# Kernel optimization log

Hardware: AMD Instinct MI355X
Metric: run time of the kernel (lower is better)

Reference implementation:

```python
import jax, jax.numpy as jnp
import numpy as np

N, IN_DIM, HID, OUT, NH = 512, 256, 256, 256, 4
HD = OUT // NH  # head_dim = 64
EPS = 1e-5


def _mlp(x, w1, b1, w2, b2):
    return jax.nn.relu(x @ w1 + b1) @ w2 + b2


def setup_inputs() -> dict:
    key = jax.random.key(0)
    ks = jax.random.split(key, 32)

    def rn(k, shape, fan_in):
        return (jax.random.normal(k, shape, jnp.float32) / np.float32(np.sqrt(fan_in)))

    V = jax.random.normal(ks[0], (N, IN_DIM), jnp.float32)
    adj = jax.random.randint(ks[1], (N, N), 0, 2, jnp.int32)
    adj = adj.at[jnp.arange(N), jnp.arange(N)].set(1)  # self-edges: avoid all -inf rows
    prev_hidden = jax.random.normal(ks[2], (N, HID), jnp.float32)
    z = jnp.zeros
    return dict(
        V=V, adj=adj, prev_hidden=prev_hidden,
        W1=rn(ks[3], (IN_DIM, HID), IN_DIM),
        a_std0=rn(ks[4], (HID, 1), HID), a_std1=rn(ks[5], (HID, 1), HID),
        ce_w1=rn(ks[6], (2 * IN_DIM, HID), 2 * IN_DIM), ce_b1=z((HID,), jnp.float32),
        ce_w2=rn(ks[7], (HID, HD), HID), ce_b2=z((HD,), jnp.float32),
        a_c0=rn(ks[8], (HD, 1), HD), a_c1=rn(ks[9], (HD, 1), HD),
        te_w1=rn(ks[10], (IN_DIM + HID, HID), IN_DIM + HID), te_b1=z((HID,), jnp.float32),
        te_w2=rn(ks[11], (HID, HD), HID), te_b2=z((HD,), jnp.float32),
        a_t0=rn(ks[12], (HD, 1), HD), a_t1=rn(ks[13], (HD, 1), HD),
        co_w1=rn(ks[14], (3 * IN_DIM, HID), 3 * IN_DIM), co_b1=z((HID,), jnp.float32),
        co_w2=rn(ks[15], (HID, HD), HID), co_b2=z((HD,), jnp.float32),
        a_co0=rn(ks[16], (HD, 1), HD), a_co1=rn(ks[17], (HD, 1), HD),
        W2=rn(ks[18], (HID + 2 * HD + 1, OUT), HID + 2 * HD + 1),
        Wo=rn(ks[19], (OUT, OUT), OUT), bo=z((OUT,), jnp.float32),
        ln_g=jnp.ones((OUT,), jnp.float32), ln_b=z((OUT,), jnp.float32),
    )


def reference(V, adj, prev_hidden, W1, a_std0, a_std1,
              ce_w1, ce_b1, ce_w2, ce_b2, a_c0, a_c1,
              te_w1, te_b1, te_w2, te_b2, a_t0, a_t1,
              co_w1, co_b1, co_w2, co_b2, a_co0, a_co1,
              W2, Wo, bo, ln_g, ln_b):
    ninf = -jnp.inf

    # ---- standard GAT branch -> H1: (N, HID) ----
    Wh1 = V @ W1
    s1 = Wh1 @ a_std0 + (Wh1 @ a_std1).T                      # (N, N)
    s1 = jnp.where(adj == 0, ninf, s1)
    H1 = jax.nn.softmax(s1, axis=1) @ Wh1

    # ---- causal branch: all ordered pairs i!=j, global softmax -> H2: (N, HD) ----
    pair = jnp.concatenate([jnp.broadcast_to(V[:, None, :], (N, N, IN_DIM)),
                            jnp.broadcast_to(V[None, :, :], (N, N, IN_DIM))], axis=-1)
    cf = _mlp(pair, ce_w1, ce_b1, ce_w2, ce_b2)               # (N, N, HD)
    cs = (cf @ (a_c0 + a_c1))[..., 0]                         # (N, N)
    cs = jnp.where(jnp.eye(N, dtype=bool), ninf, cs)          # exclude i==j pairs
    ca = jax.nn.softmax(cs.reshape(-1)).reshape(N, N, 1)
    H2 = jnp.broadcast_to((ca * cf).sum((0, 1)), (N, HD))

    # ---- temporal branch: (N,1) scores broadcast against causal mask -> running mean ----
    tf = _mlp(jnp.concatenate([V, prev_hidden], axis=-1), te_w1, te_b1, te_w2, te_b2)  # (N, HD)
    ts = tf @ (a_t0 + a_t1)                                   # (N, 1)
    cmask = jnp.triu(jnp.ones((N, N), bool), 1)
    tsb = jnp.where(cmask, ninf, jnp.broadcast_to(ts, (N, N)))
    H3 = jax.nn.softmax(tsb, axis=1) @ tf                     # (N, HD)

    # ---- coop branch: first two neighbors by index; size-1 softmax; buggy pad -> (N,1) ----
    order = jnp.argsort((1 - adj).astype(jnp.int32), axis=1, stable=True)  # adj==1 first, index order
    nb = V[order[:, :2]]                                      # (N, 2, IN_DIM)
    valid = ((adj == 1).sum(axis=1) >= 2)
    nb = jnp.where(valid[:, None, None], nb, jnp.zeros_like(nb))
    ci = jnp.concatenate([V, nb[:, 0], nb[:, 1]], axis=-1)    # (N, 3*IN_DIM)
    cf4 = _mlp(ci, co_w1, co_b1, co_w2, co_b2)                # (N, HD)
    ca4 = jax.nn.softmax(cf4 @ (a_co0 + a_co1), axis=1)       # (N,1): softmax over size-1 -> ones
    h4vec = (ca4.T @ cf4)[0]                                  # (HD,)
    # original: squeeze(-2)->(HD,), dim==1 -> unsqueeze(-1)->(HD,1), zero-pad rows to N
    H4 = jnp.zeros((N, 1), V.dtype).at[:HD, 0].set(h4vec)

    # ---- combine, lazy W2, proj, LN, ELU (dropout identity in eval) ----
    Hc = jnp.concatenate([H1, H2, H3, H4], axis=-1) @ W2      # (N, OUT)
    out = Hc @ Wo + bo
    mu = out.mean(-1, keepdims=True)
    var = ((out - mu) ** 2).mean(-1, keepdims=True)
    out = (out - mu) / jnp.sqrt(var + EPS) * ln_g + ln_b
    return jax.nn.elu(out)
```

## Files before the change

kernel.cpp:

```cpp
#include <hip/hip_runtime.h>
#include <math.h>

#define NN 512
#define HD 64
#define EPSV 1e-5f

typedef unsigned short u16;
typedef short s4v __attribute__((ext_vector_type(4)));
typedef short s8v __attribute__((ext_vector_type(8)));
typedef float f4v __attribute__((ext_vector_type(4)));

struct GD {
  const float *A, *A2, *A3, *A4;
  const int* I;
  const float *B, *bias;
  float* C;
  int M, K, Nn, mode, act;
};

#define GEMM_SMEM 28800
#define MEGA_SMEM 38656

__device__ __forceinline__ void split_bf16(float x, u16& h, u16& l) {
  unsigned xb = __float_as_uint(x);
  float hf = __uint_as_float(xb & 0xffff0000u);
  h = (u16)(xb >> 16);
  l = (u16)(__float_as_uint(x - hf) >> 16);
}

__device__ __forceinline__ void gemm_body(char* smem, const GD& d, int bx, int by) {
  u16 (*Ah)[72] = (u16(*)[72])smem;
  u16 (*Al)[72] = (u16(*)[72])(smem + 4608);
  u16 (*Bh)[68] = (u16(*)[68])(smem + 9216);
  u16 (*Bl)[68] = (u16(*)[68])(smem + 9216 + 8704);
  char* extra = smem + 26624;
  int* nbl = (int*)extra;
  float* wscl = (float*)extra;
  float* rowsuml = wscl + 512;

  const int t = threadIdx.x;
  const int rowbase = by * 32, colbase = bx * 64;
  const int K = d.K, Nn = d.Nn, mode = d.mode, M = d.M;
  if (rowbase >= M) return;

  if (mode == 2) {
    int wave = t >> 6, lane = t & 63;
    for (int rr = wave; rr < 32; rr += 4) {
      int row = rowbase + rr;
      int n0 = -1, n1 = -1, cnt = 0;
      for (int c = 0; c < 8; ++c) {
        unsigned long long mm = __ballot(d.I[row * NN + c * 64 + lane] != 0);
        cnt += (int)__popcll(mm);
        if (n0 < 0 && mm) { n0 = c * 64 + (int)__builtin_ctzll(mm); mm &= mm - 1; }
        if (n1 < 0 && mm) { n1 = c * 64 + (int)__builtin_ctzll(mm); }
      }
      if (lane == 0) { nbl[rr * 3] = n0; nbl[rr * 3 + 1] = n1; nbl[rr * 3 + 2] = (cnt >= 2); }
    }
    __syncthreads();
  } else if (mode == 4) {
    wscl[t] = d.A2[t];
    wscl[256 + t] = d.A2[256 + t];
    __syncthreads();
  }

  float4 aR[2], bR[4];
  float rs0 = 0.f, rs1 = 0.f;

  auto loadA = [&](int k0) {
#pragma unroll
    for (int j = 0; j < 2; ++j) {
      int idx = t + j * 256;
      int r = idx >> 4, c0 = (idx & 15) * 4;
      int row = rowbase + r, gk = k0 + c0;
      float4 v4 = make_float4(0.f, 0.f, 0.f, 0.f);
      if (mode == 0) {
        if (row < M && gk < K) v4 = *(const float4*)&d.A[(size_t)row * K + gk];
      } else if (mode == 1) {
        if (gk < 256) v4 = *(const float4*)&d.A[row * 256 + gk];
        else v4 = *(const float4*)&d.A2[row * 256 + gk - 256];
      } else if (mode == 2) {
        int seg = gk >> 8;
        int src = (seg == 0) ? row : (nbl[r * 3 + 2] ? nbl[r * 3 + seg - 1] : -1);
        if (src >= 0) v4 = *(const float4*)&d.A[src * 256 + (gk & 255)];
      } else if (mode == 3) {
        if (gk + 3 < 256) v4 = *(const float4*)&d.A[row * 256 + gk];
        else if (gk >= 256 && gk + 3 < 320) v4 = *(const float4*)&d.A2[gk - 256];
        else if (gk >= 320 && gk + 3 < 384) v4 = *(const float4*)&d.A3[row * 64 + gk - 320];
        else if (gk == 384) v4.x = (row < 64) ? d.A4[row] : 0.f;
      } else {
        int4 a4 = *(const int4*)&d.I[row * NN + gk];
        v4.x = a4.x ? wscl[gk + 0] : 0.f;
        v4.y = a4.y ? wscl[gk + 1] : 0.f;
        v4.z = a4.z ? wscl[gk + 2] : 0.f;
        v4.w = a4.w ? wscl[gk + 3] : 0.f;
        float ss = v4.x + v4.y + v4.z + v4.w;
        if (j == 0) rs0 += ss; else rs1 += ss;
      }
      aR[j] = v4;
    }
  };
  auto loadB = [&](int k0) {
#pragma unroll
    for (int j = 0; j < 4; ++j) {
      int idx = t + j * 256;
      int r = idx >> 4, c0 = (idx & 15) * 4;
      int gk = k0 + r;
      float4 v4 = make_float4(0.f, 0.f, 0.f, 0.f);
      if (gk < K) v4 = *(const float4*)&d.B[(size_t)gk * Nn + colbase + c0];
      bR[j] = v4;
    }
  };
  auto stos = [&]() {
#pragma unroll
    for (int j = 0; j < 2; ++j) {
      int idx = t + j * 256;
      int r = idx >> 4, c0 = (idx & 15) * 4;
      float v[4] = {aR[j].x, aR[j].y, aR[j].z, aR[j].w};
      u16 h[4], l[4];
#pragma unroll
      for (int e = 0; e < 4; ++e) split_bf16(v[e], h[e], l[e]);
      *(short4*)&Ah[r][c0] = make_short4(h[0], h[1], h[2], h[3]);
      *(short4*)&Al[r][c0] = make_short4(l[0], l[1], l[2], l[3]);
    }
#pragma unroll
    for (int j = 0; j < 4; ++j) {
      int idx = t + j * 256;
      int r = idx >> 4, c0 = (idx & 15) * 4;
      float v[4] = {bR[j].x, bR[j].y, bR[j].z, bR[j].w};
#pragma unroll
      for (int e = 0; e < 4; ++e) {
        u16 h, l;
        split_bf16(v[e], h, l);
        Bh[c0 + e][r] = h;
        Bl[c0 + e][r] = l;
      }
    }
  };

  f4v acc0 = {0.f, 0.f, 0.f, 0.f};
  f4v acc1 = {0.f, 0.f, 0.f, 0.f};

  const int w4 = t >> 6;
  const int lrow = t & 15;
  const int lk = ((t & 63) >> 4) * 8;

  int iters = (K + 63) >> 6;
  loadA(0); loadB(0);
  for (int it = 0; it < iters; ++it) {
    stos();
    __syncthreads();
    if (it + 1 < iters) { loadA((it + 1) << 6); loadB((it + 1) << 6); }
    const u16* bhrow = Bh[w4 * 16 + lrow];
    const u16* blrow = Bl[w4 * 16 + lrow];
#pragma unroll
    for (int ks = 0; ks < 2; ++ks) {
      int ko = ks * 32 + lk;
      s4v bh_0 = *(const s4v*)&bhrow[ko];
      s4v bh_1 = *(const s4v*)&bhrow[ko + 4];
      s4v bl_0 = *(const s4v*)&blrow[ko];
      s4v bl_1 = *(const s4v*)&blrow[ko + 4];
      s8v bh = __builtin_shufflevector(bh_0, bh_1, 0, 1, 2, 3, 4, 5, 6, 7);
      s8v bl = __builtin_shufflevector(bl_0, bl_1, 0, 1, 2, 3, 4, 5, 6, 7);
      {
        s8v ah = *(const s8v*)&Ah[lrow][ko];
        s8v al = *(const s8v*)&Al[lrow][ko];
        acc0 = __builtin_amdgcn_mfma_f32_16x16x32_bf16(ah, bh, acc0, 0, 0, 0);
        acc0 = __builtin_amdgcn_mfma_f32_16x16x32_bf16(ah, bl, acc0, 0, 0, 0);
        acc0 = __builtin_amdgcn_mfma_f32_16x16x32_bf16(al, bh, acc0, 0, 0, 0);
      }
      {
        s8v ah = *(const s8v*)&Ah[16 + lrow][ko];
        s8v al = *(const s8v*)&Al[16 + lrow][ko];
        acc1 = __builtin_amdgcn_mfma_f32_16x16x32_bf16(ah, bh, acc1, 0, 0, 0);
        acc1 = __builtin_amdgcn_mfma_f32_16x16x32_bf16(ah, bl, acc1, 0, 0, 0);
        acc1 = __builtin_amdgcn_mfma_f32_16x16x32_bf16(al, bh, acc1, 0, 0, 0);
      }
    }
    __syncthreads();
  }

  if (mode == 4) {
    float a0 = rs0, a1 = rs1;
#pragma unroll
    for (int off = 8; off; off >>= 1) {
      a0 += __shfl_xor(a0, off, 16);
      a1 += __shfl_xor(a1, off, 16);
    }
    if ((t & 15) == 0) { rowsuml[t >> 4] = a0; rowsuml[16 + (t >> 4)] = a1; }
    __syncthreads();
  }

  int col = colbase + w4 * 16 + lrow;
  float bvs = d.bias ? d.bias[col] : 0.f;
  int qrow = ((t & 63) >> 4) * 4;
#pragma unroll
  for (int m = 0; m < 2; ++m) {
#pragma unroll
    for (int q = 0; q < 4; ++q) {
      int lr = m * 16 + qrow + q;
      int row = rowbase + lr;
      if (row >= M) continue;
      float o = (m ? acc1[q] : acc0[q]) + bvs;
      if (d.act) o = fmaxf(o, 0.f);
      if (mode == 4) o *= (1.f / rowsuml[lr]);
      d.C[(size_t)row * Nn + col] = o;
    }
  }
}

__device__ void wsc_body(char* smem, const float* W1, const float* a_std1,
                         const float* V, float* expwsc, int grp) {
  float* asl = (float*)smem;
  float* ul  = asl + 256;
  int t = threadIdx.x;
  asl[t] = a_std1[t];
  __syncthreads();
  {
    float s = 0.f;
    const float* wr = W1 + t * 256;
    for (int h = 0; h < 256; h += 4) {
      float4 w4 = *(const float4*)&wr[h];
      float4 a4 = *(const float4*)&asl[h];
      s += w4.x * a4.x + w4.y * a4.y + w4.z * a4.z + w4.w * a4.w;
    }
    ul[t] = s;
  }
  __syncthreads();
  int wave = t >> 6, lane = t & 63;
  float4 u4 = *(const float4*)&ul[lane * 4];
  int j0 = grp * 128;
  for (int j = j0 + wave; j < j0 + 128; j += 4) {
    float4 v4 = *(const float4*)&V[j * 256 + lane * 4];
    float s = v4.x * u4.x + v4.y * u4.y + v4.z * u4.z + v4.w * u4.w;
#pragma unroll
    for (int off = 32; off; off >>= 1) s += __shfl_xor(s, off, 64);
    if (lane == 0) expwsc[j] = __expf(s);
  }
}

struct GD7 { GD d[7]; };
__global__ __launch_bounds__(256) void gemm7_k(GD7 ds) {
  __shared__ __align__(16) char smem[GEMM_SMEM];
  int z = blockIdx.z;
  if (z == 6) {
    if (blockIdx.y != 0) return;
    wsc_body(smem, ds.d[6].A, ds.d[6].A2, ds.d[6].A3, ds.d[6].C, blockIdx.x);
    return;
  }
  gemm_body(smem, ds.d[z], blockIdx.x, blockIdx.y);
}
__global__ __launch_bounds__(256) void gemm1_k(GD d) {
  __shared__ __align__(16) char smem[GEMM_SMEM];
  gemm_body(smem, d, blockIdx.x, blockIdx.y);
}

__device__ void pair_body(char* smem,
    const float* __restrict__ P, const float* __restrict__ Q,
    const float* __restrict__ b1, const float* __restrict__ ce_w2,
    const float* __restrict__ a_c0, const float* __restrict__ a_c1,
    float* __restrict__ mpart, float* __restrict__ dpart,
    float* __restrict__ spart, int byy, int bxx) {
  float* Pl  = (float*)smem;
  float* Ql  = Pl + 16 * 260;
  float* el  = Ql + 16 * 260;
  float* wcl = el + 16 * 20;
  float* red = wcl + 256;
  float* sk  = red + 256;
  float* sbl = sk + 256;
  int t = threadIdx.x;

  if (t < 64) red[t] = a_c0[t] + a_c1[t];
  __syncthreads();
  {
    float s = 0.f;
    const float* w2r = ce_w2 + t * 64;
#pragma unroll 8
    for (int h = 0; h < 64; ++h) s += w2r[h] * red[h];
    wcl[t] = s;
  }
  int i0 = byy * 16, j0 = bxx * 16;
  for (int e = t; e < 1024; e += 256) {
    int r = e >> 6, c4 = (e & 63) * 4;
    float4 bb = *(const float4*)&b1[c4];
    float4 pv = *(const float4*)&P[(i0 + r) * 256 + c4];
    pv.x += bb.x; pv.y += bb.y; pv.z += bb.z; pv.w += bb.w;
    *(float4*)&Pl[r * 260 + c4] = pv;
    *(float4*)&Ql[r * 260 + c4] = *(const float4*)&Q[(j0 + r) * 256 + c4];
  }
  __syncthreads();

  int a = t >> 4, b = t & 15;
  const float* pr = &Pl[a * 260];
  const float* qr = &Ql[b * 260];
  float4 c4a = make_float4(0.f, 0.f, 0.f, 0.f);
#pragma unroll 8
  for (int k4 = 0; k4 < 64; ++k4) {
    float4 w = *(const float4*)&wcl[k4 * 4];
    float4 p = *(const float4*)&pr[k4 * 4];
    float4 q = *(const float4*)&qr[k4 * 4];
    c4a.x += fmaxf(p.x + q.x, 0.f) * w.x;
    c4a.y += fmaxf(p.y + q.y, 0.f) * w.y;
    c4a.z += fmaxf(p.z + q.z, 0.f) * w.z;
    c4a.w += fmaxf(p.w + q.w, 0.f) * w.w;
  }
  float s = c4a.x + c4a.y + c4a.z + c4a.w;
  if (i0 + a == j0 + b) s = -INFINITY;
  red[t] = s; __syncthreads();
  for (int ss = 128; ss; ss >>= 1) { if (t < ss) red[t] = fmaxf(red[t], red[t + ss]); __syncthreads(); }
  float mb = red[0];
  __syncthreads();
  float e = __expf(s - mb);
  el[a * 20 + b] = e;
  red[t] = e; __syncthreads();
  for (int ss = 128; ss; ss >>= 1) { if (t < ss) red[t] += red[t + ss]; __syncthreads(); }
  float db = red[0];
  __syncthreads();

  float qv[16];
#pragma unroll
  for (int j = 0; j < 16; ++j) qv[j] = Ql[j * 260 + t];
  float rk = 0.f;
#pragma unroll 4
  for (int i = 0; i < 16; ++i) {
    float pv = Pl[i * 260 + t];
    const float* erow = &el[i * 20];
#pragma unroll
    for (int j4 = 0; j4 < 4; ++j4) {
      float4 e4 = *(const float4*)&erow[j4 * 4];
      rk += e4.x * fmaxf(pv + qv[j4 * 4 + 0], 0.f);
      rk += e4.y * fmaxf(pv + qv[j4 * 4 + 1], 0.f);
      rk += e4.z * fmaxf(pv + qv[j4 * 4 + 2], 0.f);
      rk += e4.w * fmaxf(pv + qv[j4 * 4 + 3], 0.f);
    }
  }
  sk[t] = rk;
  __syncthreads();
  {
    int h = t & 63, q = t >> 6;
    float s2 = 0.f;
    for (int k = q * 64; k < q * 64 + 64; ++k) s2 += sk[k] * ce_w2[k * 64 + h];
    sbl[q * 64 + h] = s2;
  }
  __syncthreads();
  int blk = byy * 32 + bxx;
  if (t < 64) spart[blk * 64 + t] = sbl[t] + sbl[64 + t] + sbl[128 + t] + sbl[192 + t];
  if (t == 0) { mpart[blk] = mb; dpart[blk] = db; }
}

struct MegaArgs {
  const float *P, *Q, *b1, *ce_w2, *a_c0, *a_c1;
  float *mpart, *dpart, *spart;
  GD gH1, gTf, gCf;
};

__global__ __launch_bounds__(256) void mega_k(MegaArgs a) {
  __shared__ __align__(16) char smem[MEGA_SMEM];
  int b = blockIdx.x;
  if (b < 64) {
    gemm_body(smem, a.gH1, b & 3, b >> 2);
  } else if (b < 80) {
    gemm_body(smem, a.gTf, 0, b - 64);
  } else if (b < 96) {
    gemm_body(smem, a.gCf, 0, b - 80);
  } else {
    int p = b - 96;
    pair_body(smem, a.P, a.Q, a.b1, a.ce_w2, a.a_c0, a.a_c1,
              a.mpart, a.dpart, a.spart, p >> 5, p & 31);
  }
}

__global__ __launch_bounds__(1024) void mini_k(
    const float* __restrict__ mpart, const float* __restrict__ dpart,
    const float* __restrict__ spart, const float* __restrict__ ce_b2,
    float* __restrict__ H2row,
    const float* __restrict__ tf, float* __restrict__ H3,
    const float* __restrict__ cf4, float* __restrict__ h4vec) {
  __shared__ float A[1024];
  __shared__ float Bsh[1024];
  __shared__ float segsum[16][65];
  int b = blockIdx.x, t = threadIdx.x;
  if (b == 0) {
    float mv = mpart[t];
    A[t] = mv; __syncthreads();
    for (int s = 512; s; s >>= 1) { if (t < s) A[t] = fmaxf(A[t], A[t + s]); __syncthreads(); }
    float M = A[0];
    __syncthreads();
    float e = __expf(mv - M);
    Bsh[t] = e;
    A[t] = e * dpart[t];
    __syncthreads();
    for (int s = 512; s; s >>= 1) { if (t < s) A[t] += A[t + s]; __syncthreads(); }
    float D = A[0];
    __syncthreads();
    int h = t & 63, g = t >> 6;
    float s2 = 0.f;
    for (int b2 = g * 64; b2 < g * 64 + 64; ++b2) s2 += Bsh[b2] * spart[b2 * 64 + h];
    A[t] = s2;
    __syncthreads();
    for (int p = 8; p; p >>= 1) { if (g < p) A[g * 64 + h] += A[(g + p) * 64 + h]; __syncthreads(); }
    if (t < 64) H2row[t] = A[t] / D + ce_b2[t];
  } else if (b == 1) {
    int h = t & 63, g = t >> 6;
    float vals[32];
    float run = 0.f;
#pragma unroll
    for (int r = 0; r < 32; ++r) { run += tf[(g * 32 + r) * 64 + h]; vals[r] = run; }
    segsum[g][h] = run;
    __syncthreads();
    float off = 0.f;
    for (int gg = 0; gg < g; ++gg) off += segsum[gg][h];
#pragma unroll
    for (int r = 0; r < 32; ++r) {
      int i = g * 32 + r;
      H3[i * 64 + h] = (vals[r] + off) / (float)(i + 1);
    }
  } else {
    int h = t & 63, g = t >> 6;
    float s = 0.f;
    for (int r = 0; r < 32; ++r) s += cf4[(g * 32 + r) * 64 + h];
    A[g * 64 + h] = s;
    __syncthreads();
    for (int p = 8; p; p >>= 1) { if (g < p) A[g * 64 + h] += A[(g + p) * 64 + h]; __syncthreads(); }
    if (t < 64) h4vec[t] = A[t];
  }
}

__global__ void ln_elu_kernel(const float* __restrict__ X, const float* __restrict__ g,
                              const float* __restrict__ b, float* __restrict__ out) {
  __shared__ float red[256];
  int i = blockIdx.x, tid = threadIdx.x;
  float x = X[i * 256 + tid];
  red[tid] = x; __syncthreads();
  for (int s = 128; s; s >>= 1) { if (tid < s) red[tid] += red[tid + s]; __syncthreads(); }
  float mu = red[0] * (1.f / 256.f);
  __syncthreads();
  float d = x - mu;
  red[tid] = d * d; __syncthreads();
  for (int s = 128; s; s >>= 1) { if (tid < s) red[tid] += red[tid + s]; __syncthreads(); }
  float var = red[0] * (1.f / 256.f);
  float y = d / sqrtf(var + EPSV) * g[tid] + b[tid];
  out[i * 256 + tid] = (y > 0.f) ? y : (expf(y) - 1.f);
}

static GD mkgd(const float* A, const float* A2, const float* A3, const float* A4,
               const int* I, const float* B, const float* bias, float* C,
               int M, int K, int Nn, int mode, int act) {
  GD g{A, A2, A3, A4, I, B, bias, C, M, K, Nn, mode, act};
  return g;
}

extern "C" void kernel_launch(void* const* d_in, const int* in_sizes, int n_in,
                              void* d_out, int out_size, void* d_ws, size_t ws_size,
                              hipStream_t stream) {
  const float* V      = (const float*)d_in[0];
  const int*   adj    = (const int*)  d_in[1];
  const float* ph     = (const float*)d_in[2];
  const float* W1     = (const float*)d_in[3];
  const float* a_std1 = (const float*)d_in[5];
  const float* ce_w1  = (const float*)d_in[6];
  const float* ce_b1  = (const float*)d_in[7];
  const float* ce_w2  = (const float*)d_in[8];
  const float* ce_b2  = (const float*)d_in[9];
  const float* a_c0   = (const float*)d_in[10];
  const float* a_c1   = (const float*)d_in[11];
  const float* te_w1  = (const float*)d_in[12];
  const float* te_b1  = (const float*)d_in[13];
  const float* te_w2  = (const float*)d_in[14];
  const float* te_b2  = (const float*)d_in[15];
  const float* co_w1  = (const float*)d_in[18];
  const float* co_b1  = (const float*)d_in[19];
  const float* co_w2  = (const float*)d_in[20];
  const float* co_b2  = (const float*)d_in[21];
  const float* W2     = (const float*)d_in[24];
  const float* Wo     = (const float*)d_in[25];
  const float* bo     = (const float*)d_in[26];
  const float* ln_g   = (const float*)d_in[27];
  const float* ln_b   = (const float*)d_in[28];
  float* out = (float*)d_out;

  float* ws = (float*)d_ws;
  size_t off = 0;
  auto alloc = [&](size_t n) { float* p = ws + off; off += (n + 15) & ~(size_t)15; return p; };

  float* Wh1    = alloc(512 * 256);
  float* Pb     = alloc(512 * 256);
  float* Qb     = alloc(512 * 256);
  float* tfh    = alloc(512 * 256);
  float* cf4h   = alloc(512 * 256);
  float* H1     = alloc(512 * 256);
  float* Wfused = alloc(385 * 256);
  float* T2     = alloc(512 * 256);
  float* tf     = alloc(512 * 64);
  float* cf4    = alloc(512 * 64);
  float* H3     = alloc(512 * 64);
  float* spart  = alloc(1024 * 64);
  float* mpart  = alloc(1024);
  float* dpart  = alloc(1024);
  float* expwsc = alloc(512);
  float* H2row  = alloc(64);
  float* h4vec  = alloc(64);
  (void)ws_size; (void)in_sizes; (void)n_in; (void)out_size;

  GD7 sA;
  sA.d[0] = mkgd(V, 0, 0, 0, 0, W1, 0, Wh1, 512, 256, 256, 0, 0);
  sA.d[1] = mkgd(V, 0, 0, 0, 0, ce_w1, 0, Pb, 512, 256, 256, 0, 0);
  sA.d[2] = mkgd(V, 0, 0, 0, 0, ce_w1 + 256 * 256, 0, Qb, 512, 256, 256, 0, 0);
  sA.d[3] = mkgd(V, ph, 0, 0, 0, te_w1, te_b1, tfh, 512, 512, 256, 1, 1);
  sA.d[4] = mkgd(V, 0, 0, 0, adj, co_w1, co_b1, cf4h, 512, 768, 256, 2, 1);
  sA.d[5] = mkgd(W2, 0, 0, 0, 0, Wo, 0, Wfused, 385, 256, 256, 0, 0);
  sA.d[6] = mkgd(W1, a_std1, V, 0, 0, 0, 0, expwsc, 512, 256, 1, 6, 0);
  gemm7_k<<<dim3(4, 16, 7), 256, 0, stream>>>(sA);

  MegaArgs ma;
  ma.P = Pb; ma.Q = Qb; ma.b1 = ce_b1; ma.ce_w2 = ce_w2;
  ma.a_c0 = a_c0; ma.a_c1 = a_c1;
  ma.mpart = mpart; ma.dpart = dpart; ma.spart = spart;
  ma.gH1 = mkgd(0, expwsc, 0, 0, adj, Wh1, 0, H1, 512, 512, 256, 4, 0);
  ma.gTf = mkgd(tfh, 0, 0, 0, 0, te_w2, te_b2, tf, 512, 256, 64, 0, 0);
  ma.gCf = mkgd(cf4h, 0, 0, 0, 0, co_w2, co_b2, cf4, 512, 256, 64, 0, 0);
  mega_k<<<1120, 256, 0, stream>>>(ma);

  mini_k<<<3, 1024, 0, stream>>>(mpart, dpart, spart, ce_b2, H2row, tf, H3, cf4, h4vec);

  GD gF = mkgd(H1, H2row, H3, h4vec, 0, Wfused, bo, T2, 512, 385, 256, 3, 0);
  gemm1_k<<<dim3(4, 16), 256, 0, stream>>>(gF);

  ln_elu_kernel<<<512, 256, 0, stream>>>(T2, ln_g, ln_b, out);
}
```

Measured before the change: 193.7 us.

## Pre-split B operands into transposed bf16 hi/lo buffers for downstream GEMMs

The producer GEMMs for Wh1 and the fused W2·Wo weight now write their outputs as transposed bf16 high/low halves. A new conversion block in the first launch does the same for te_w2 and co_w2. Consumer GEMMs then load these pre-split, k-contiguous operands with wide vector loads and copy them straight into shared memory, skipping the per-tile float-to-bf16 split and the strided transposed stores. Separately, the pair kernel reads a precomputed ce_w2·(a_c0+a_c1) vector and uses wave-shuffle reductions instead of shared-memory tree reductions. The costs are extra workspace, a padded fused-weight layout that relies on zero padding, and unguarded row writes in the transposed epilogue.

```diff
diff --git a/kernel.cpp b/kernel.cpp
--- a/kernel.cpp
+++ b/kernel.cpp
@@ -15,6 +15,9 @@
   const int* I;
   const float *B, *bias;
   float* C;
+  const u16 *Bth, *Btl;
+  u16 *Cth, *Ctl;
+  int Bkp, Ckp;
   int M, K, Nn, mode, act;
 };
 
@@ -64,6 +67,7 @@
   }
 
   float4 aR[2], bR[4];
+  s8v bp[4];
   float rs0 = 0.f, rs1 = 0.f;
 
   auto loadA = [&](int k0) {
@@ -100,14 +104,25 @@
     }
   };
   auto loadB = [&](int k0) {
-#pragma unroll
-    for (int j = 0; j < 4; ++j) {
-      int idx = t + j * 256;
-      int r = idx >> 4, c0 = (idx & 15) * 4;
-      int gk = k0 + r;
-      float4 v4 = make_float4(0.f, 0.f, 0.f, 0.f);
-      if (gk < K) v4 = *(const float4*)&d.B[(size_t)gk * Nn + colbase + c0];
-      bR[j] = v4;
+    if (d.Bth) {
+#pragma unroll
+      for (int j = 0; j < 2; ++j) {
+        int idx = t + j * 256;
+        int n = idx >> 3, kb = (idx & 7) * 8;
+        size_t base = (size_t)(colbase + n) * d.Bkp + k0 + kb;
+        bp[j] = *(const s8v*)&d.Bth[base];
+        bp[2 + j] = *(const s8v*)&d.Btl[base];
+      }
+    } else {
+#pragma unroll
+      for (int j = 0; j < 4; ++j) {
+        int idx = t + j * 256;
+        int r = idx >> 4, c0 = (idx & 15) * 4;
+        int gk = k0 + r;
+        float4 v4 = make_float4(0.f, 0.f, 0.f, 0.f);
+        if (gk < K) v4 = *(const float4*)&d.B[(size_t)gk * Nn + colbase + c0];
+        bR[j] = v4;
+      }
     }
   };
   auto stos = [&]() {
@@ -119,20 +134,30 @@
       u16 h[4], l[4];
 #pragma unroll
       for (int e = 0; e < 4; ++e) split_bf16(v[e], h[e], l[e]);
-      *(short4*)&Ah[r][c0] = make_short4(h[0], h[1], h[2], h[3]);
-      *(short4*)&Al[r][c0] = make_short4(l[0], l[1], l[2], l[3]);
-    }
-#pragma unroll
-    for (int j = 0; j < 4; ++j) {
-      int idx = t + j * 256;
-      int r = idx >> 4, c0 = (idx & 15) * 4;
-      float v[4] = {bR[j].x, bR[j].y, bR[j].z, bR[j].w};
-#pragma unroll
-      for (int e = 0; e < 4; ++e) {
-        u16 h, l;
-        split_bf16(v[e], h, l);
-        Bh[c0 + e][r] = h;
-        Bl[c0 + e][r] = l;
+      *(short4*)&Ah[r][c0] = make_short4((short)h[0], (short)h[1], (short)h[2], (short)h[3]);
+      *(short4*)&Al[r][c0] = make_short4((short)l[0], (short)l[1], (short)l[2], (short)l[3]);
+    }
+    if (d.Bth) {
+#pragma unroll
+      for (int j = 0; j < 2; ++j) {
+        int idx = t + j * 256;
+        int n = idx >> 3, kb = (idx & 7) * 8;
+        *(s8v*)&Bh[n][kb] = bp[j];
+        *(s8v*)&Bl[n][kb] = bp[2 + j];
+      }
+    } else {
+#pragma unroll
+      for (int j = 0; j < 4; ++j) {
+        int idx = t + j * 256;
+        int r = idx >> 4, c0 = (idx & 15) * 4;
+        float v[4] = {bR[j].x, bR[j].y, bR[j].z, bR[j].w};
+#pragma unroll
+        for (int e = 0; e < 4; ++e) {
+          u16 h, l;
+          split_bf16(v[e], h, l);
+          Bh[c0 + e][r] = h;
+          Bl[c0 + e][r] = l;
+        }
       }
     }
   };
@@ -191,19 +216,32 @@
   }
 
   int col = colbase + w4 * 16 + lrow;
-  float bvs = d.bias ? d.bias[col] : 0.f;
   int qrow = ((t & 63) >> 4) * 4;
-#pragma unroll
-  for (int m = 0; m < 2; ++m) {
-#pragma unroll
-    for (int q = 0; q < 4; ++q) {
-      int lr = m * 16 + qrow + q;
-      int row = rowbase + lr;
-      if (row >= M) continue;
-      float o = (m ? acc1[q] : acc0[q]) + bvs;
-      if (d.act) o = fmaxf(o, 0.f);
-      if (mode == 4) o *= (1.f / rowsuml[lr]);
-      d.C[(size_t)row * Nn + col] = o;
+  if (d.Cth) {
+    size_t cb = (size_t)col * d.Ckp + rowbase + qrow;
+#pragma unroll
+    for (int m = 0; m < 2; ++m) {
+      u16 hh[4], ll[4];
+#pragma unroll
+      for (int q = 0; q < 4; ++q) split_bf16(m ? acc1[q] : acc0[q], hh[q], ll[q]);
+      *(short4*)&d.Cth[cb + m * 16] = make_short4((short)hh[0], (short)hh[1], (short)hh[2], (short)hh[3]);
+      *(short4*)&d.Ctl[cb + m * 16] = make_short4((short)ll[0], (short)ll[1], (short)ll[2], (short)ll[3]);
+    }
+  }
+  if (d.C) {
+    float bvs = d.bias ? d.bias[col] : 0.f;
+#pragma unroll
+    for (int m = 0; m < 2; ++m) {
+#pragma unroll
+      for (int q = 0; q < 4; ++q) {
+        int lr = m * 16 + qrow + q;
+        int row = rowbase + lr;
+        if (row >= M) continue;
+        float o = (m ? acc1[q] : acc0[q]) + bvs;
+        if (d.act) o = fmaxf(o, 0.f);
+        if (mode == 4) o *= (1.f / rowsuml[lr]);
+        d.C[(size_t)row * Nn + col] = o;
+      }
     }
   }
 }
@@ -238,13 +276,60 @@
   }
 }
 
-struct GD7 { GD d[7]; };
+struct GD7 {
+  GD d[7];
+  const float *tw2, *cw2, *ce_w2, *a_c0, *a_c1;
+  u16 *tw2h, *tw2l, *cw2h, *cw2l, *wfh, *wfl;
+  float* wclg;
+};
+
+__device__ void conv_body(char* smem, int bx, const GD7& a) {
+  float (*Ls)[66] = (float(*)[66])smem;
+  int t = threadIdx.x;
+  const float* src = (bx < 2) ? a.tw2 : a.cw2;
+  u16* dh = (bx < 2) ? a.tw2h : a.cw2h;
+  u16* dl = (bx < 2) ? a.tw2l : a.cw2l;
+  int k0 = (bx & 1) * 128;
+  for (int kt = 0; kt < 2; ++kt) {
+    int k00 = k0 + kt * 64;
+#pragma unroll
+    for (int j = 0; j < 4; ++j) {
+      int idx = t + j * 256;
+      int r = idx >> 4, c = (idx & 15) * 4;
+      *(float4*)&Ls[r][c] = *(const float4*)&src[(k00 + r) * 64 + c];
+    }
+    __syncthreads();
+#pragma unroll
+    for (int j = 0; j < 4; ++j) {
+      int idx = t + j * 256;
+      int n = idx >> 4, kk = (idx & 15) * 4;
+      u16 hh[4], ll[4];
+#pragma unroll
+      for (int e = 0; e < 4; ++e) split_bf16(Ls[kk + e][n], hh[e], ll[e]);
+      *(short4*)&dh[n * 256 + k00 + kk] = make_short4((short)hh[0], (short)hh[1], (short)hh[2], (short)hh[3]);
+      *(short4*)&dl[n * 256 + k00 + kk] = make_short4((short)ll[0], (short)ll[1], (short)ll[2], (short)ll[3]);
+    }
+    __syncthreads();
+  }
+  if (bx == 3) {
+    float s = 0.f;
+    const float* w2r = a.ce_w2 + t * 64;
+    for (int h = 0; h < 64; ++h) s += w2r[h] * (a.a_c0[h] + a.a_c1[h]);
+    a.wclg[t] = s;
+    int n = t;
+    for (int kk = 416; kk < 448; kk += 4) {
+      *(short4*)&a.wfh[n * 448 + kk] = make_short4(0, 0, 0, 0);
+      *(short4*)&a.wfl[n * 448 + kk] = make_short4(0, 0, 0, 0);
+    }
+  }
+}
+
 __global__ __launch_bounds__(256) void gemm7_k(GD7 ds) {
   __shared__ __align__(16) char smem[GEMM_SMEM];
   int z = blockIdx.z;
   if (z == 6) {
-    if (blockIdx.y != 0) return;
-    wsc_body(smem, ds.d[6].A, ds.d[6].A2, ds.d[6].A3, ds.d[6].C, blockIdx.x);
+    if (blockIdx.y == 0) { wsc_body(smem, ds.d[6].A, ds.d[6].A2, ds.d[6].A3, ds.d[6].C, blockIdx.x); return; }
+    if (blockIdx.y == 1) { conv_body(smem, blockIdx.x, ds); return; }
     return;
   }
   gemm_body(smem, ds.d[z], blockIdx.x, blockIdx.y);
@@ -257,7 +342,7 @@
 __device__ void pair_body(char* smem,
     const float* __restrict__ P, const float* __restrict__ Q,
     const float* __restrict__ b1, const float* __restrict__ ce_w2,
-    const float* __restrict__ a_c0, const float* __restrict__ a_c1,
+    const float* __restrict__ wclg,
     float* __restrict__ mpart, float* __restrict__ dpart,
     float* __restrict__ spart, int byy, int bxx) {
   float* Pl  = (float*)smem;
@@ -269,15 +354,7 @@
   float* sbl = sk + 256;
   int t = threadIdx.x;
 
-  if (t < 64) red[t] = a_c0[t] + a_c1[t];
-  __syncthreads();
-  {
-    float s = 0.f;
-    const float* w2r = ce_w2 + t * 64;
-#pragma unroll 8
-    for (int h = 0; h < 64; ++h) s += w2r[h] * red[h];
-    wcl[t] = s;
-  }
+  wcl[t] = wclg[t];
   int i0 = byy * 16, j0 = bxx * 16;
   for (int e = t; e < 1024; e += 256) {
     int r = e >> 6, c4 = (e & 63) * 4;
@@ -305,16 +382,20 @@
   }
   float s = c4a.x + c4a.y + c4a.z + c4a.w;
   if (i0 + a == j0 + b) s = -INFINITY;
-  red[t] = s; __syncthreads();
-  for (int ss = 128; ss; ss >>= 1) { if (t < ss) red[t] = fmaxf(red[t], red[t + ss]); __syncthreads(); }
-  float mb = red[0];
-  __syncthreads();
+  float wm = s;
+#pragma unroll
+  for (int off = 32; off; off >>= 1) wm = fmaxf(wm, __shfl_xor(wm, off, 64));
+  if ((t & 63) == 0) red[t >> 6] = wm;
+  __syncthreads();
+  float mb = fmaxf(fmaxf(red[0], red[1]), fmaxf(red[2], red[3]));
   float e = __expf(s - mb);
   el[a * 20 + b] = e;
-  red[t] = e; __syncthreads();
-  for (int ss = 128; ss; ss >>= 1) { if (t < ss) red[t] += red[t + ss]; __syncthreads(); }
-  float db = red[0];
-  __syncthreads();
+  float ws2 = e;
+#pragma unroll
+  for (int off = 32; off; off >>= 1) ws2 += __shfl_xor(ws2, off, 64);
+  if ((t & 63) == 0) red[8 + (t >> 6)] = ws2;
+  __syncthreads();
+  float db = red[8] + red[9] + red[10] + red[11];
 
   float qv[16];
 #pragma unroll
@@ -348,7 +429,7 @@
 }
 
 struct MegaArgs {
-  const float *P, *Q, *b1, *ce_w2, *a_c0, *a_c1;
+  const float *P, *Q, *b1, *ce_w2, *wclg;
   float *mpart, *dpart, *spart;
   GD gH1, gTf, gCf;
 };
@@ -364,7 +445,7 @@
     gemm_body(smem, a.gCf, 0, b - 80);
   } else {
     int p = b - 96;
-    pair_body(smem, a.P, a.Q, a.b1, a.ce_w2, a.a_c0, a.a_c1,
+    pair_body(smem, a.P, a.Q, a.b1, a.ce_w2, a.wclg,
               a.mpart, a.dpart, a.spart, p >> 5, p & 31);
   }
 }
@@ -445,7 +526,7 @@
 static GD mkgd(const float* A, const float* A2, const float* A3, const float* A4,
                const int* I, const float* B, const float* bias, float* C,
                int M, int K, int Nn, int mode, int act) {
-  GD g{A, A2, A3, A4, I, B, bias, C, M, K, Nn, mode, act};
+  GD g{A, A2, A3, A4, I, B, bias, C, 0, 0, 0, 0, 0, 0, M, K, Nn, mode, act};
   return g;
 }
 
@@ -482,13 +563,11 @@
   size_t off = 0;
   auto alloc = [&](size_t n) { float* p = ws + off; off += (n + 15) & ~(size_t)15; return p; };
 
-  float* Wh1    = alloc(512 * 256);
   float* Pb     = alloc(512 * 256);
   float* Qb     = alloc(512 * 256);
   float* tfh    = alloc(512 * 256);
   float* cf4h   = alloc(512 * 256);
   float* H1     = alloc(512 * 256);
-  float* Wfused = alloc(385 * 256);
   float* T2     = alloc(512 * 256);
   float* tf     = alloc(512 * 64);
   float* cf4    = alloc(512 * 64);
@@ -499,30 +578,47 @@
   float* expwsc = alloc(512);
   float* H2row  = alloc(64);
   float* h4vec  = alloc(64);
+  u16* Wh1t_h = (u16*)alloc(65536);
+  u16* Wh1t_l = (u16*)alloc(65536);
+  u16* Wf_h   = (u16*)alloc(57344);
+  u16* Wf_l   = (u16*)alloc(57344);
+  u16* tw2h   = (u16*)alloc(8192);
+  u16* tw2l   = (u16*)alloc(8192);
+  u16* cw2h   = (u16*)alloc(8192);
+  u16* cw2l   = (u16*)alloc(8192);
+  float* wclg = alloc(256);
   (void)ws_size; (void)in_sizes; (void)n_in; (void)out_size;
 
   GD7 sA;
-  sA.d[0] = mkgd(V, 0, 0, 0, 0, W1, 0, Wh1, 512, 256, 256, 0, 0);
+  sA.d[0] = mkgd(V, 0, 0, 0, 0, W1, 0, 0, 512, 256, 256, 0, 0);
+  sA.d[0].Cth = Wh1t_h; sA.d[0].Ctl = Wh1t_l; sA.d[0].Ckp = 512;
   sA.d[1] = mkgd(V, 0, 0, 0, 0, ce_w1, 0, Pb, 512, 256, 256, 0, 0);
   sA.d[2] = mkgd(V, 0, 0, 0, 0, ce_w1 + 256 * 256, 0, Qb, 512, 256, 256, 0, 0);
   sA.d[3] = mkgd(V, ph, 0, 0, 0, te_w1, te_b1, tfh, 512, 512, 256, 1, 1);
   sA.d[4] = mkgd(V, 0, 0, 0, adj, co_w1, co_b1, cf4h, 512, 768, 256, 2, 1);
-  sA.d[5] = mkgd(W2, 0, 0, 0, 0, Wo, 0, Wfused, 385, 256, 256, 0, 0);
+  sA.d[5] = mkgd(W2, 0, 0, 0, 0, Wo, 0, 0, 385, 256, 256, 0, 0);
+  sA.d[5].Cth = Wf_h; sA.d[5].Ctl = Wf_l; sA.d[5].Ckp = 448;
   sA.d[6] = mkgd(W1, a_std1, V, 0, 0, 0, 0, expwsc, 512, 256, 1, 6, 0);
+  sA.tw2 = te_w2; sA.cw2 = co_w2; sA.ce_w2 = ce_w2; sA.a_c0 = a_c0; sA.a_c1 = a_c1;
+  sA.tw2h = tw2h; sA.tw2l = tw2l; sA.cw2h = cw2h; sA.cw2l = cw2l;
+  sA.wfh = Wf_h; sA.wfl = Wf_l; sA.wclg = wclg;
   gemm7_k<<<dim3(4, 16, 7), 256, 0, stream>>>(sA);
 
   MegaArgs ma;
-  ma.P = Pb; ma.Q = Qb; ma.b1 = ce_b1; ma.ce_w2 = ce_w2;
-  ma.a_c0 = a_c0; ma.a_c1 = a_c1;
+  ma.P = Pb; ma.Q = Qb; ma.b1 = ce_b1; ma.ce_w2 = ce_w2; ma.wclg = wclg;
   ma.mpart = mpart; ma.dpart = dpart; ma.spart = spart;
-  ma.gH1 = mkgd(0, expwsc, 0, 0, adj, Wh1, 0, H1, 512, 512, 256, 4, 0);
-  ma.gTf = mkgd(tfh, 0, 0, 0, 0, te_w2, te_b2, tf, 512, 256, 64, 0, 0);
-  ma.gCf = mkgd(cf4h, 0, 0, 0, 0, co_w2, co_b2, cf4, 512, 256, 64, 0, 0);
+  ma.gH1 = mkgd(0, expwsc, 0, 0, adj, 0, 0, H1, 512, 512, 256, 4, 0);
+  ma.gH1.Bth = Wh1t_h; ma.gH1.Btl = Wh1t_l; ma.gH1.Bkp = 512;
+  ma.gTf = mkgd(tfh, 0, 0, 0, 0, 0, te_b2, tf, 512, 256, 64, 0, 0);
+  ma.gTf.Bth = tw2h; ma.gTf.Btl = tw2l; ma.gTf.Bkp = 256;
+  ma.gCf = mkgd(cf4h, 0, 0, 0, 0, 0, co_b2, cf4, 512, 256, 64, 0, 0);
+  ma.gCf.Bth = cw2h; ma.gCf.Btl = cw2l; ma.gCf.Bkp = 256;
   mega_k<<<1120, 256, 0, stream>>>(ma);
 
   mini_k<<<3, 1024, 0, stream>>>(mpart, dpart, spart, ce_b2, H2row, tf, H3, cf4, h4vec);
 
-  GD gF = mkgd(H1, H2row, H3, h4vec, 0, Wfused, bo, T2, 512, 385, 256, 3, 0);
+  GD gF = mkgd(H1, H2row, H3, h4vec, 0, 0, bo, T2, 512, 385, 256, 3, 0);
+  gF.Bth = Wf_h; gF.Btl = Wf_l; gF.Bkp = 448;
   gemm1_k<<<dim3(4, 16), 256, 0, stream>>>(gF);
 
   ln_elu_kernel<<<512, 256, 0, stream>>>(T2, ln_g, ln_b, out);
```

Result: no change. 191.2 us, median of 2 (-1.3%).
